# Performance work log

Measured on AMD Instinct MI355X. Metric: run time of the kernel, lower is better.

The kernel has to match this reference:

```python
import jax, jax.numpy as jnp
import numpy as np
import math

N_EMBD = 1024
N_HEAD = 16
B, T = 2, 2048
MASK_VAL = -10.0  # non-standard soft mask value from original module


def setup_inputs() -> dict:
    key = jax.random.key(0)
    k1, k2, k3 = jax.random.split(key, 3)
    scale = 1.0 / math.sqrt(N_EMBD)
    x = jax.random.normal(k1, (B, T, N_EMBD), dtype=jnp.float32)
    # torch Linear weights: (out_features, in_features)
    w_attn = jax.random.normal(k2, (3 * N_EMBD, N_EMBD), dtype=jnp.float32) * scale
    w_proj = jax.random.normal(k3, (N_EMBD, N_EMBD), dtype=jnp.float32) * scale
    return {"x": x, "w_attn": w_attn, "w_proj": w_proj}


def reference(x, w_attn, w_proj):
    Bsz, Tlen, C = x.shape
    hs = C // N_HEAD
    qkv = jnp.einsum('btc,fc->btf', x, w_attn)  # [B,T,3C]
    q, k, v = jnp.split(qkv, 3, axis=-1)
    # [B,H,T,hs]
    q = q.reshape(Bsz, Tlen, N_HEAD, hs).transpose(0, 2, 1, 3)
    k = k.reshape(Bsz, Tlen, N_HEAD, hs).transpose(0, 2, 1, 3)
    v = v.reshape(Bsz, Tlen, N_HEAD, hs).transpose(0, 2, 1, 3)
    att = jnp.einsum('bhqd,bhkd->bhqk', q, k) * (1.0 / math.sqrt(hs))
    causal = jnp.tril(jnp.ones((Tlen, Tlen), dtype=bool))
    att = jnp.where(causal[None, None], att, MASK_VAL)
    att = jax.nn.softmax(att, axis=-1)
    y = jnp.einsum('bhqk,bhkd->bhqd', att, v)
    y = y.transpose(0, 2, 1, 3).reshape(Bsz, Tlen, C)
    return jnp.einsum('btc,fc->btf', y, w_proj)
```

## Files before the change

kernel.cpp:

```cpp
#include <hip/hip_runtime.h>
#include <hip/hip_bf16.h>
#include <stdint.h>

#define BSZ   2
#define TT    2048
#define NH    16
#define HS    64
#define CC    1024
#define C3    3072
#define MT    4096
#define E10   4.5399929762484854e-05f
#define SCL2  0.1803368801111204f

typedef __bf16 bf16;
typedef __bf16 bf16x8 __attribute__((ext_vector_type(8)));
typedef float  f32x4  __attribute__((ext_vector_type(4)));
typedef short  s16x4  __attribute__((ext_vector_type(4)));

#define AS1 __attribute__((address_space(1)))
#define AS3 __attribute__((address_space(3)))

__device__ __forceinline__ void glds16(const bf16* g, bf16* l) {
    __builtin_amdgcn_global_load_lds((const AS1 void*)g, (AS3 void*)l, 16, 0, 0);
}

#define NX8  (MT * CC / 8)
#define NWA8 (C3 * CC / 8)
#define NWP8 (CC * CC / 8)
__global__ __launch_bounds__(256)
void convert_all(const float* __restrict__ x, const float* __restrict__ wa,
                 const float* __restrict__ wp, bf16* __restrict__ xd,
                 bf16* __restrict__ wad, bf16* __restrict__ wpd,
                 int* __restrict__ flag) {
    __shared__ int wsum[4];
    const int tid = threadIdx.x;
    const uint16_t* x16 = (const uint16_t*)x;
    int local = 0;
    {
        uint16_t u = x16[tid];
        int e = (u >> 7) & 0xFF; local += (e >= 96 && e <= 159);
        u = x16[tid + 256];
        e = (u >> 7) & 0xFF; local += (e >= 96 && e <= 159);
    }
    local += __shfl_xor(local, 1, 64);
    local += __shfl_xor(local, 2, 64);
    local += __shfl_xor(local, 4, 64);
    local += __shfl_xor(local, 8, 64);
    local += __shfl_xor(local, 16, 64);
    local += __shfl_xor(local, 32, 64);
    if ((tid & 63) == 0) wsum[tid >> 6] = local;
    __syncthreads();
    const int cnt = wsum[0] + wsum[1] + wsum[2] + wsum[3];
    const int f = (cnt >= 461) ? 0 : 1;
    if (blockIdx.x == 0 && tid == 0) *flag = f;
    if (f == 0) return;

    long i = (long)blockIdx.x * 256 + tid;
    const float* s; bf16* d; long off;
    if (i < NX8)             { s = x;  d = xd;  off = i; }
    else if (i < NX8 + NWA8) { s = wa; d = wad; off = i - NX8; }
    else                     { s = wp; d = wpd; off = i - NX8 - NWA8; }
    const float4* sp = reinterpret_cast<const float4*>(s) + off * 2;
    float4 a = sp[0], b = sp[1];
    bf16x8 r;
    r[0] = (bf16)a.x; r[1] = (bf16)a.y; r[2] = (bf16)a.z; r[3] = (bf16)a.w;
    r[4] = (bf16)b.x; r[5] = (bf16)b.y; r[6] = (bf16)b.z; r[7] = (bf16)b.w;
    reinterpret_cast<bf16x8*>(d)[off] = r;
}

__global__ __launch_bounds__(256)
void gemm_bt(const bf16* __restrict__ A0, const bf16* __restrict__ A1,
             const bf16* __restrict__ B0, const bf16* __restrict__ B1,
             void* __restrict__ Cmain, bf16* __restrict__ Cv,
             float* __restrict__ Vtile,
             const int* __restrict__ flag,
             int M, int N, int K, int lda, int ldb, int ldc,
             int split_col, int cf32_dyn) {
    __shared__ __align__(16) char smem[33792];
    bf16* As0 = (bf16*)smem;
    bf16* Bs0 = (bf16*)(smem + 16384);

    const int f = *flag;
    const bf16* A = f ? A1 : A0;
    const bf16* B = f ? B1 : B0;
    const int cf32 = cf32_dyn & f;

    const int tid  = threadIdx.x;
    const int lane = tid & 63;
    const int wave = tid >> 6;
    const int wm   = wave >> 1;
    const int wn   = wave & 1;
    const int quad = lane >> 4;
    const int l16  = lane & 15;

    const int row0 = blockIdx.y * 128;
    const int col0 = blockIdx.x * 128;
    const bool mainblk = (split_col < 0 || col0 < split_col);

    const int srow = tid >> 2;
    const int skk  = (tid & 3) * 8;

    const bf16* Ap = A + (long)(row0 + srow) * lda + skk;
    const bf16* Bp = B + (long)(col0 + srow) * ldb + skk;

    auto stage = [&](int k0, int buf) {
        glds16(Ap + k0,                  As0 + buf * 4096 + wave * 512);
        glds16(Ap + (long)64 * lda + k0, As0 + buf * 4096 + wave * 512 + 2048);
        glds16(Bp + k0,                  Bs0 + buf * 4096 + wave * 512);
        glds16(Bp + (long)64 * ldb + k0, Bs0 + buf * 4096 + wave * 512 + 2048);
    };

    f32x4 acc[4][4] = {};
    stage(0, 0);

    for (int k0 = 0; k0 < K; k0 += 32) {
        const int buf = (k0 >> 5) & 1;
        __syncthreads();
        if (k0 + 32 < K) stage(k0 + 32, buf ^ 1);

        const bf16* Ac = As0 + buf * 4096;
        const bf16* Bc = Bs0 + buf * 4096;
        bf16x8 af[4], bfv[4];
#pragma unroll
        for (int mi = 0; mi < 4; ++mi)
            af[mi] = *reinterpret_cast<const bf16x8*>(&Ac[(wm * 64 + mi * 16 + l16) * 32 + quad * 8]);
#pragma unroll
        for (int ni = 0; ni < 4; ++ni)
            bfv[ni] = *reinterpret_cast<const bf16x8*>(&Bc[(wn * 64 + ni * 16 + l16) * 32 + quad * 8]);
#pragma unroll
        for (int mi = 0; mi < 4; ++mi)
#pragma unroll
            for (int ni = 0; ni < 4; ++ni)
                acc[mi][ni] = __builtin_amdgcn_mfma_f32_16x16x32_bf16(af[mi], bfv[ni], acc[mi][ni], 0, 0, 0);
    }

    if (mainblk) {
        if (cf32) {
#pragma unroll
            for (int mi = 0; mi < 4; ++mi)
#pragma unroll
                for (int ni = 0; ni < 4; ++ni)
#pragma unroll
                    for (int r = 0; r < 4; ++r) {
                        int row = row0 + wm * 64 + mi * 16 + quad * 4 + r;
                        int col = col0 + wn * 64 + ni * 16 + l16;
                        ((float*)Cmain)[(long)row * ldc + col] = acc[mi][ni][r];
                    }
        } else {
            __syncthreads();
            bf16* Ce = (bf16*)smem;
#pragma unroll
            for (int mi = 0; mi < 4; ++mi) {
                const int row = wm * 64 + mi * 16 + quad * 4;
#pragma unroll
                for (int ni = 0; ni < 4; ++ni) {
                    const int col = wn * 64 + ni * 16 + l16;
#pragma unroll
                    for (int r = 0; r < 4; ++r)
                        Ce[(row + r) * 132 + col] = (bf16)acc[mi][ni][r];
                }
            }
            __syncthreads();
            const int prow = tid >> 4;
            const int pc   = (tid & 15) * 8;
#pragma unroll
            for (int p = 0; p < 8; ++p) {
                const int row_l = p * 16 + prow;
                uint2 w0 = *reinterpret_cast<const uint2*>(&Ce[row_l * 132 + pc]);
                uint2 w1 = *reinterpret_cast<const uint2*>(&Ce[row_l * 132 + pc + 4]);
                uint4 w; w.x = w0.x; w.y = w0.y; w.z = w1.x; w.w = w1.y;
                *reinterpret_cast<uint4*>(
                    (bf16*)Cmain + (long)(row0 + row_l) * ldc + col0 + pc) = w;
            }
        }
    } else {
        const int h  = (col0 - split_col + wn * 64) >> 6;
        const int bq = row0 >> 11;
        const int tc = ((row0 & 2047) >> 6) + wm;
#pragma unroll
        for (int ni = 0; ni < 4; ++ni) {
            long vrow = (long)(bq * NH + h) * 64 + ni * 16 + l16;
#pragma unroll
            for (int mi = 0; mi < 4; ++mi) {
                bf16 outv[4];
#pragma unroll
                for (int r = 0; r < 4; ++r) outv[r] = (bf16)acc[mi][ni][r];
                *reinterpret_cast<uint2*>(&Cv[vrow * 2048 + tc * 64 + quad * 16 + mi * 4]) =
                    *reinterpret_cast<uint2*>(outv);
            }
        }
#pragma unroll
        for (int ni = 0; ni < 4; ++ni) {
            float s = 0.f;
#pragma unroll
            for (int mi = 0; mi < 4; ++mi)
#pragma unroll
                for (int r = 0; r < 4; ++r) s += acc[mi][ni][r];
            s += __shfl_xor(s, 16, 64);
            s += __shfl_xor(s, 32, 64);
            if (quad == 0)
                Vtile[((long)(bq * NH + h) * 32 + tc) * 64 + ni * 16 + l16] = s;
        }
    }
}

__global__ __launch_bounds__(256)
void gemm_bt64(const bf16* __restrict__ A0, const bf16* __restrict__ A1,
               const bf16* __restrict__ B0, const bf16* __restrict__ B1,
               void* __restrict__ C, const int* __restrict__ flag,
               int M, int N, int K, int lda, int ldb, int ldc, int cf32_dyn) {
    __shared__ bf16 As[2][128 * 32];
    __shared__ bf16 Bs[2][64 * 32];

    const int f = *flag;
    const bf16* A = f ? A1 : A0;
    const bf16* B = f ? B1 : B0;
    const int cf32 = cf32_dyn & f;

    const int tid  = threadIdx.x;
    const int lane = tid & 63;
    const int wave = tid >> 6;
    const int wm   = wave >> 1;
    const int wn   = wave & 1;
    const int quad = lane >> 4;
    const int l16  = lane & 15;

    const int row0 = blockIdx.y * 128;
    const int col0 = blockIdx.x * 64;

    const int srow = tid >> 2;
    const int skk  = (tid & 3) * 8;

    const bf16* Ap = A + (long)(row0 + srow) * lda + skk;
    const bf16* Bp = B + (long)(col0 + srow) * ldb + skk;

    auto stage = [&](int k0, int buf) {
        glds16(Ap + k0,                  &As[buf][wave * 512]);
        glds16(Ap + (long)64 * lda + k0, &As[buf][wave * 512 + 2048]);
        glds16(Bp + k0,                  &Bs[buf][wave * 512]);
    };

    f32x4 acc[4][2] = {};
    stage(0, 0);

    for (int k0 = 0; k0 < K; k0 += 32) {
        const int buf = (k0 >> 5) & 1;
        __syncthreads();
        if (k0 + 32 < K) stage(k0 + 32, buf ^ 1);

        const bf16* Ac = As[buf];
        const bf16* Bc = Bs[buf];
        bf16x8 af[4], bfv[2];
#pragma unroll
        for (int mi = 0; mi < 4; ++mi)
            af[mi] = *reinterpret_cast<const bf16x8*>(&Ac[(wm * 64 + mi * 16 + l16) * 32 + quad * 8]);
#pragma unroll
        for (int ni = 0; ni < 2; ++ni)
            bfv[ni] = *reinterpret_cast<const bf16x8*>(&Bc[(wn * 32 + ni * 16 + l16) * 32 + quad * 8]);
#pragma unroll
        for (int mi = 0; mi < 4; ++mi)
#pragma unroll
            for (int ni = 0; ni < 2; ++ni)
                acc[mi][ni] = __builtin_amdgcn_mfma_f32_16x16x32_bf16(af[mi], bfv[ni], acc[mi][ni], 0, 0, 0);
    }

#pragma unroll
    for (int mi = 0; mi < 4; ++mi)
#pragma unroll
        for (int ni = 0; ni < 2; ++ni)
#pragma unroll
            for (int r = 0; r < 4; ++r) {
                int row = row0 + wm * 64 + mi * 16 + quad * 4 + r;
                int col = col0 + wn * 32 + ni * 16 + l16;
                float v = acc[mi][ni][r];
                if (cf32) ((float*)C)[(long)row * ldc + col] = v;
                else      ((bf16*)C)[(long)row * ldc + col] = (bf16)v;
            }
}

__global__ __launch_bounds__(256, 3)
void attn(bf16* __restrict__ qk, const bf16* __restrict__ Vt,
          const float* __restrict__ Vtile) {
    __shared__ bf16 Ks[3][64 * 64];
    __shared__ bf16 Vs[3][64 * 64];
    __shared__ float Vpart[4][64];

    const int tid  = threadIdx.x;
    const int lane = tid & 63;
    const int wave = tid >> 6;
    const int quad = lane >> 4;
    const int l16  = lane & 15;

    const int f2   = blockIdx.x;
    const int xcd  = f2 & 7;
    const int slot = f2 >> 3;
    const int u    = slot & 3;
    const int chunk = 31 - (slot >> 2);
    const int h = xcd * 2 + (u & 1);
    const int b = u >> 1;
    const int bh = b * 16 + h;
    const int q0 = chunk * 64;
    const long rbase = (long)b * TT;
    const int ktend = chunk + 1;

    const bf16* qp = qk + (rbase + q0 + wave * 16 + l16) * 2048 + h * HS;
    bf16x8 qf0 = *reinterpret_cast<const bf16x8*>(qp + quad * 8);
    bf16x8 qf1 = *reinterpret_cast<const bf16x8*>(qp + 32 + quad * 8);
#pragma unroll
    for (int j = 0; j < 8; ++j) {
        qf0[j] = (bf16)((float)qf0[j] * SCL2);
        qf1[j] = (bf16)((float)qf1[j] * SCL2);
    }

    f32x4 O[4] = {};
    f32x4 lpacc = {};
    const short one_bf16 = (short)0x3F80;
    const s16x4 ones = {one_bf16, one_bf16, one_bf16, one_bf16};

    const int rl  = lane >> 3;
    const int cs  = (lane & 7) ^ rl;
    const int row0dma = wave * 16 + rl;
    const bf16* kgb = qk + (rbase + row0dma) * 2048 + CC + h * HS + cs * 8;
    const bf16* vgb = Vt + ((long)(b * NH + h) * 64 + row0dma) * 2048 + cs * 8;
    const int sx = l16 & 7;

    auto stage = [&](int kt, int bi) {
        glds16(kgb + (long)(kt * 64) * 2048,     &Ks[bi][wave * 1024]);
        glds16(kgb + (long)(kt * 64 + 8) * 2048, &Ks[bi][wave * 1024 + 512]);
        glds16(vgb + kt * 64,                    &Vs[bi][wave * 1024]);
        glds16(vgb + 8 * 2048 + kt * 64,         &Vs[bi][wave * 1024 + 512]);
    };

    auto qkTile = [&](int bi, f32x4* Sn) {
        const bf16* Kc = Ks[bi];
        bf16x8 kf0[4], kf1[4];
#pragma unroll
        for (int g = 0; g < 4; ++g) {
            const int krow = g * 16 + l16;
            kf0[g] = *reinterpret_cast<const bf16x8*>(&Kc[krow * 64 + ((quad ^ sx) * 8)]);
            kf1[g] = *reinterpret_cast<const bf16x8*>(&Kc[krow * 64 + (((4 + quad) ^ sx) * 8)]);
        }
        __builtin_amdgcn_s_setprio(1);
#pragma unroll
        for (int g = 0; g < 4; ++g) {
            Sn[g] = __builtin_amdgcn_mfma_f32_16x16x32_bf16(kf0[g], qf0, Sn[g], 0, 0, 0);
            Sn[g] = __builtin_amdgcn_mfma_f32_16x16x32_bf16(kf1[g], qf1, Sn[g], 0, 0, 0);
        }
        __builtin_amdgcn_s_setprio(0);
    };
    auto vTile = [&](int bi, s16x4 vf[4][4]) {
        const bf16* Vc = Vs[bi];
#pragma unroll
        for (int dg = 0; dg < 4; ++dg) {
            const int vrow = dg * 16 + l16;
            union { uint4 u4; s16x4 s[2]; } ua, ub;
            ua.u4 = *reinterpret_cast<const uint4*>(&Vc[vrow * 64 + (((2 * quad) ^ sx) * 8)]);
            ub.u4 = *reinterpret_cast<const uint4*>(&Vc[vrow * 64 + (((2 * quad + 1) ^ sx) * 8)]);
            vf[dg][0] = ua.s[0]; vf[dg][1] = ua.s[1];
            vf[dg][2] = ub.s[0]; vf[dg][3] = ub.s[1];
        }
    };

    stage(0, 0);
    stage(ktend > 1 ? 1 : 0, 1);
    asm volatile("s_waitcnt vmcnt(4)" ::: "memory");
    __builtin_amdgcn_s_barrier();
    __builtin_amdgcn_sched_barrier(0);

    f32x4 Sc[4] = {};
    s16x4 vc[4][4] = {};
    qkTile(0, Sc);
    vTile(0, vc);

    int rb = 1;
    int sb = 2;
    for (int kt = 0; kt < ktend; ++kt) {
        int nkt = kt + 2; nkt = (nkt < ktend) ? nkt : (ktend - 1);
        stage(nkt, sb);
        asm volatile("s_waitcnt vmcnt(4)" ::: "memory");
        __builtin_amdgcn_s_barrier();
        __builtin_amdgcn_sched_barrier(0);

        f32x4 Sn[4] = {};
        s16x4 vn[4][4] = {};
        if (kt + 1 < ktend) {
            qkTile(rb, Sn);
            vTile(rb, vn);
        }

        const bool dtile = (kt == ktend - 1);
        const int ql = wave * 16 + l16;
        s16x4 pk[4];
#pragma unroll
        for (int g = 0; g < 4; ++g) {
#pragma unroll
            for (int r = 0; r < 4; ++r) {
                float p = __builtin_exp2f(Sc[g][r]);
                if (dtile) {
                    int kl = g * 16 + quad * 4 + r;
                    p = (kl > ql) ? E10 : p;
                }
                union { bf16 b_; short s_; } u2;
                u2.b_ = (bf16)p;
                pk[g][r] = u2.s_;
            }
        }

        __builtin_amdgcn_s_setprio(1);
#pragma unroll
        for (int dg = 0; dg < 4; ++dg) {
            O[dg] = __builtin_amdgcn_mfma_f32_16x16x16bf16_1k(vc[dg][0], pk[0], O[dg], 0, 0, 0);
            O[dg] = __builtin_amdgcn_mfma_f32_16x16x16bf16_1k(vc[dg][1], pk[1], O[dg], 0, 0, 0);
            O[dg] = __builtin_amdgcn_mfma_f32_16x16x16bf16_1k(vc[dg][2], pk[2], O[dg], 0, 0, 0);
            O[dg] = __builtin_amdgcn_mfma_f32_16x16x16bf16_1k(vc[dg][3], pk[3], O[dg], 0, 0, 0);
        }
        lpacc = __builtin_amdgcn_mfma_f32_16x16x16bf16_1k(ones, pk[0], lpacc, 0, 0, 0);
        lpacc = __builtin_amdgcn_mfma_f32_16x16x16bf16_1k(ones, pk[1], lpacc, 0, 0, 0);
        lpacc = __builtin_amdgcn_mfma_f32_16x16x16bf16_1k(ones, pk[2], lpacc, 0, 0, 0);
        lpacc = __builtin_amdgcn_mfma_f32_16x16x16bf16_1k(ones, pk[3], lpacc, 0, 0, 0);
        __builtin_amdgcn_s_setprio(0);

#pragma unroll
        for (int g = 0; g < 4; ++g) Sc[g] = Sn[g];
#pragma unroll
        for (int dg = 0; dg < 4; ++dg)
#pragma unroll
            for (int j = 0; j < 4; ++j) vc[dg][j] = vn[dg][j];

        rb = (rb == 2) ? 0 : rb + 1;
        sb = (sb == 2) ? 0 : sb + 1;
    }

    {
        float s = 0.f;
        for (int kt = ktend + wave; kt < 32; kt += 4)
            s += Vtile[((long)bh * 32 + kt) * 64 + lane];
        Vpart[wave][lane] = s;
    }
    __syncthreads();

    const int nfut = TT - ktend * 64;
    const float l = lpacc[0] + (float)nfut * E10;
    const float invl = 1.0f / l;

    bf16* yp = qk + (rbase + q0 + wave * 16 + l16) * 2048 + h * HS;
#pragma unroll
    for (int dg = 0; dg < 4; ++dg) {
        bf16 outv[4];
#pragma unroll
        for (int r = 0; r < 4; ++r) {
            const int d = dg * 16 + quad * 4 + r;
            float vts = Vpart[0][d] + Vpart[1][d] + Vpart[2][d] + Vpart[3][d];
            float o = O[dg][r] + E10 * vts;
            outv[r] = (bf16)(o * invl);
        }
        *reinterpret_cast<uint2*>(yp + dg * 16 + quad * 4) =
            *reinterpret_cast<uint2*>(outv);
    }
}

extern "C" void kernel_launch(void* const* d_in, const int* in_sizes, int n_in,
                              void* d_out, int out_size, void* d_ws, size_t ws_size,
                              hipStream_t stream) {
    const void* x      = d_in[0];
    const void* w_attn = d_in[1];
    const void* w_proj = d_in[2];

    char* ws = (char*)d_ws;
    bf16*  qk     = (bf16*)ws;
    bf16*  Vt     = (bf16*)(ws + (size_t)MT * 2048 * 2);
    char*  p2     = ws + (size_t)MT * 2048 * 2 + (size_t)32 * 64 * 2048 * 2;
    int*   flag   = (int*)p2;
    bf16*  wp_cvt = (bf16*)(p2 + 256 + 32 * 33 * 64 * 4);
    float* Vtile  = (float*)((char*)wp_cvt + (size_t)CC * CC * 2);

    bf16* x_cvt  = (bf16*)d_out;
    bf16* wa_cvt = (bf16*)d_out + (size_t)MT * CC;

    convert_all<<<(NX8 + NWA8 + NWP8) / 256, 256, 0, stream>>>(
        (const float*)x, (const float*)w_attn, (const float*)w_proj,
        x_cvt, wa_cvt, wp_cvt, flag);

    gemm_bt<<<dim3(C3 / 128, MT / 128), 256, 0, stream>>>(
        (const bf16*)x, x_cvt, (const bf16*)w_attn, wa_cvt, qk, Vt, Vtile, flag,
        MT, C3, CC, CC, CC, 2048, 2048, 0);

    attn<<<dim3(1024), 256, 0, stream>>>(qk, Vt, Vtile);

    gemm_bt64<<<dim3(CC / 64, MT / 128), 256, 0, stream>>>(
        qk, qk, (const bf16*)w_proj, wp_cvt, d_out, flag,
        MT, CC, CC, 2048, CC, CC, 1);
}
```

Before: 175.6 us.

## Stage fp32 GEMM epilogue through LDS and ping-pong attention register buffers

Result: faster. 170.8 us (-2.7%).

```diff
diff --git a/kernel.cpp b/kernel.cpp
--- a/kernel.cpp
+++ b/kernel.cpp
@@ -209,8 +209,9 @@
                const bf16* __restrict__ B0, const bf16* __restrict__ B1,
                void* __restrict__ C, const int* __restrict__ flag,
                int M, int N, int K, int lda, int ldb, int ldc, int cf32_dyn) {
-    __shared__ bf16 As[2][128 * 32];
-    __shared__ bf16 Bs[2][64 * 32];
+    __shared__ __align__(16) char smem[34816];
+    bf16* As0 = (bf16*)smem;
+    bf16* Bs0 = (bf16*)(smem + 16384);
 
     const int f = *flag;
     const bf16* A = f ? A1 : A0;
@@ -235,9 +236,9 @@
     const bf16* Bp = B + (long)(col0 + srow) * ldb + skk;
 
     auto stage = [&](int k0, int buf) {
-        glds16(Ap + k0,                  &As[buf][wave * 512]);
-        glds16(Ap + (long)64 * lda + k0, &As[buf][wave * 512 + 2048]);
-        glds16(Bp + k0,                  &Bs[buf][wave * 512]);
+        glds16(Ap + k0,                  As0 + buf * 4096 + wave * 512);
+        glds16(Ap + (long)64 * lda + k0, As0 + buf * 4096 + wave * 512 + 2048);
+        glds16(Bp + k0,                  Bs0 + buf * 2048 + wave * 512);
     };
 
     f32x4 acc[4][2] = {};
@@ -248,8 +249,8 @@
         __syncthreads();
         if (k0 + 32 < K) stage(k0 + 32, buf ^ 1);
 
-        const bf16* Ac = As[buf];
-        const bf16* Bc = Bs[buf];
+        const bf16* Ac = As0 + buf * 4096;
+        const bf16* Bc = Bs0 + buf * 2048;
         bf16x8 af[4], bfv[2];
 #pragma unroll
         for (int mi = 0; mi < 4; ++mi)
@@ -264,18 +265,42 @@
                 acc[mi][ni] = __builtin_amdgcn_mfma_f32_16x16x32_bf16(af[mi], bfv[ni], acc[mi][ni], 0, 0, 0);
     }
 
-#pragma unroll
-    for (int mi = 0; mi < 4; ++mi)
-#pragma unroll
-        for (int ni = 0; ni < 2; ++ni)
-#pragma unroll
-            for (int r = 0; r < 4; ++r) {
-                int row = row0 + wm * 64 + mi * 16 + quad * 4 + r;
-                int col = col0 + wn * 32 + ni * 16 + l16;
-                float v = acc[mi][ni][r];
-                if (cf32) ((float*)C)[(long)row * ldc + col] = v;
-                else      ((bf16*)C)[(long)row * ldc + col] = (bf16)v;
+    if (cf32) {
+        __syncthreads();
+        float* Ce = (float*)smem;
+#pragma unroll
+        for (int mi = 0; mi < 4; ++mi) {
+            const int row = wm * 64 + mi * 16 + quad * 4;
+#pragma unroll
+            for (int ni = 0; ni < 2; ++ni) {
+                const int col = wn * 32 + ni * 16 + l16;
+#pragma unroll
+                for (int r = 0; r < 4; ++r)
+                    Ce[(row + r) * 68 + col] = acc[mi][ni][r];
             }
+        }
+        __syncthreads();
+        const int prow = tid >> 4;
+        const int pcf  = (tid & 15) * 4;
+#pragma unroll
+        for (int p = 0; p < 8; ++p) {
+            const int row_l = p * 16 + prow;
+            f32x4 w = *reinterpret_cast<const f32x4*>(&Ce[row_l * 68 + pcf]);
+            *reinterpret_cast<f32x4*>(
+                (float*)C + (long)(row0 + row_l) * ldc + col0 + pcf) = w;
+        }
+    } else {
+#pragma unroll
+        for (int mi = 0; mi < 4; ++mi)
+#pragma unroll
+            for (int ni = 0; ni < 2; ++ni)
+#pragma unroll
+                for (int r = 0; r < 4; ++r) {
+                    int row = row0 + wm * 64 + mi * 16 + quad * 4 + r;
+                    int col = col0 + wn * 32 + ni * 16 + l16;
+                    ((bf16*)C)[(long)row * ldc + col] = (bf16)acc[mi][ni][r];
+                }
+    }
 }
 
 __global__ __launch_bounds__(256, 3)
@@ -316,6 +341,7 @@
     f32x4 lpacc = {};
     const short one_bf16 = (short)0x3F80;
     const s16x4 ones = {one_bf16, one_bf16, one_bf16, one_bf16};
+    const f32x4 FZ = {0.f, 0.f, 0.f, 0.f};
 
     const int rl  = lane >> 3;
     const int cs  = (lane & 7) ^ rl;
@@ -331,7 +357,7 @@
         glds16(vgb + 8 * 2048 + kt * 64,         &Vs[bi][wave * 1024 + 512]);
     };
 
-    auto qkTile = [&](int bi, f32x4* Sn) {
+    auto qkTile = [&](int bi, f32x4 (&Sn)[4]) {
         const bf16* Kc = Ks[bi];
         bf16x8 kf0[4], kf1[4];
 #pragma unroll
@@ -343,12 +369,12 @@
         __builtin_amdgcn_s_setprio(1);
 #pragma unroll
         for (int g = 0; g < 4; ++g) {
-            Sn[g] = __builtin_amdgcn_mfma_f32_16x16x32_bf16(kf0[g], qf0, Sn[g], 0, 0, 0);
+            Sn[g] = __builtin_amdgcn_mfma_f32_16x16x32_bf16(kf0[g], qf0, FZ, 0, 0, 0);
             Sn[g] = __builtin_amdgcn_mfma_f32_16x16x32_bf16(kf1[g], qf1, Sn[g], 0, 0, 0);
         }
         __builtin_amdgcn_s_setprio(0);
     };
-    auto vTile = [&](int bi, s16x4 vf[4][4]) {
+    auto vTile = [&](int bi, s16x4 (&vf)[4][4]) {
         const bf16* Vc = Vs[bi];
 #pragma unroll
         for (int dg = 0; dg < 4; ++dg) {
@@ -361,31 +387,20 @@
         }
     };
 
-    stage(0, 0);
-    stage(ktend > 1 ? 1 : 0, 1);
-    asm volatile("s_waitcnt vmcnt(4)" ::: "memory");
-    __builtin_amdgcn_s_barrier();
-    __builtin_amdgcn_sched_barrier(0);
-
-    f32x4 Sc[4] = {};
-    s16x4 vc[4][4] = {};
-    qkTile(0, Sc);
-    vTile(0, vc);
-
-    int rb = 1;
-    int sb = 2;
-    for (int kt = 0; kt < ktend; ++kt) {
+    f32x4 SA[4], SB[4];
+    s16x4 vA[4][4], vB[4][4];
+
+    auto body = [&](int kt, f32x4 (&Scur)[4], s16x4 (&vcur)[4][4],
+                    f32x4 (&Snxt)[4], s16x4 (&vnxt)[4][4]) {
         int nkt = kt + 2; nkt = (nkt < ktend) ? nkt : (ktend - 1);
-        stage(nkt, sb);
+        stage(nkt, (kt + 2) % 3);
         asm volatile("s_waitcnt vmcnt(4)" ::: "memory");
         __builtin_amdgcn_s_barrier();
         __builtin_amdgcn_sched_barrier(0);
 
-        f32x4 Sn[4] = {};
-        s16x4 vn[4][4] = {};
         if (kt + 1 < ktend) {
-            qkTile(rb, Sn);
-            vTile(rb, vn);
+            qkTile((kt + 1) % 3, Snxt);
+            vTile((kt + 1) % 3, vnxt);
         }
 
         const bool dtile = (kt == ktend - 1);
@@ -395,7 +410,7 @@
         for (int g = 0; g < 4; ++g) {
 #pragma unroll
             for (int r = 0; r < 4; ++r) {
-                float p = __builtin_exp2f(Sc[g][r]);
+                float p = __builtin_exp2f(Scur[g][r]);
                 if (dtile) {
                     int kl = g * 16 + quad * 4 + r;
                     p = (kl > ql) ? E10 : p;
@@ -409,32 +424,38 @@
         __builtin_amdgcn_s_setprio(1);
 #pragma unroll
         for (int dg = 0; dg < 4; ++dg) {
-            O[dg] = __builtin_amdgcn_mfma_f32_16x16x16bf16_1k(vc[dg][0], pk[0], O[dg], 0, 0, 0);
-            O[dg] = __builtin_amdgcn_mfma_f32_16x16x16bf16_1k(vc[dg][1], pk[1], O[dg], 0, 0, 0);
-            O[dg] = __builtin_amdgcn_mfma_f32_16x16x16bf16_1k(vc[dg][2], pk[2], O[dg], 0, 0, 0);
-            O[dg] = __builtin_amdgcn_mfma_f32_16x16x16bf16_1k(vc[dg][3], pk[3], O[dg], 0, 0, 0);
+            O[dg] = __builtin_amdgcn_mfma_f32_16x16x16bf16_1k(vcur[dg][0], pk[0], O[dg], 0, 0, 0);
+            O[dg] = __builtin_amdgcn_mfma_f32_16x16x16bf16_1k(vcur[dg][1], pk[1], O[dg], 0, 0, 0);
+            O[dg] = __builtin_amdgcn_mfma_f32_16x16x16bf16_1k(vcur[dg][2], pk[2], O[dg], 0, 0, 0);
+            O[dg] = __builtin_amdgcn_mfma_f32_16x16x16bf16_1k(vcur[dg][3], pk[3], O[dg], 0, 0, 0);
         }
         lpacc = __builtin_amdgcn_mfma_f32_16x16x16bf16_1k(ones, pk[0], lpacc, 0, 0, 0);
         lpacc = __builtin_amdgcn_mfma_f32_16x16x16bf16_1k(ones, pk[1], lpacc, 0, 0, 0);
         lpacc = __builtin_amdgcn_mfma_f32_16x16x16bf16_1k(ones, pk[2], lpacc, 0, 0, 0);
         lpacc = __builtin_amdgcn_mfma_f32_16x16x16bf16_1k(ones, pk[3], lpacc, 0, 0, 0);
         __builtin_amdgcn_s_setprio(0);
-
-#pragma unroll
-        for (int g = 0; g < 4; ++g) Sc[g] = Sn[g];
-#pragma unroll
-        for (int dg = 0; dg < 4; ++dg)
-#pragma unroll
-            for (int j = 0; j < 4; ++j) vc[dg][j] = vn[dg][j];
-
-        rb = (rb == 2) ? 0 : rb + 1;
-        sb = (sb == 2) ? 0 : sb + 1;
+    };
+
+    stage(0, 0);
+    stage(ktend > 1 ? 1 : 0, 1);
+    asm volatile("s_waitcnt vmcnt(4)" ::: "memory");
+    __builtin_amdgcn_s_barrier();
+    __builtin_amdgcn_sched_barrier(0);
+    qkTile(0, SA);
+    vTile(0, vA);
+
+    int kt = 0;
+    while (true) {
+        body(kt, SA, vA, SB, vB);
+        if (++kt >= ktend) break;
+        body(kt, SB, vB, SA, vA);
+        if (++kt >= ktend) break;
     }
 
     {
         float s = 0.f;
-        for (int kt = ktend + wave; kt < 32; kt += 4)
-            s += Vtile[((long)bh * 32 + kt) * 64 + lane];
+        for (int k2 = ktend + wave; k2 < 32; k2 += 4)
+            s += Vtile[((long)bh * 32 + k2) * 64 + lane];
         Vpart[wave][lane] = s;
     }
     __syncthreads();
```
